# Kernel optimization log

Hardware: AMD Instinct MI355X
Metric: run time of the kernel (lower is better)

The kernel has to match this reference:

```python
import jax, jax.numpy as jnp
import numpy as np

D_MODEL = 1024
NUM_HEADS = 16
D_K = D_MODEL // NUM_HEADS
B, T = 2, 2048
NEG = -1e9


def setup_inputs() -> dict:
    key = jax.random.key(0)
    ks = jax.random.split(key, 12)
    s = 1.0 / np.sqrt(D_MODEL)
    q = jax.random.normal(ks[0], (B, T, D_MODEL), jnp.float32)
    k = jax.random.normal(ks[1], (B, T, D_MODEL), jnp.float32)
    v = jax.random.normal(ks[2], (B, T, D_MODEL), jnp.float32)
    # padding mask: True = valid key; realistic per-example lengths
    lengths = jnp.array([T, 3 * T // 4], dtype=jnp.int32)
    key_padding_mask = jnp.arange(T)[None, :] < lengths[:, None]
    Wq = jax.random.uniform(ks[3], (D_MODEL, D_MODEL), jnp.float32, -s, s)
    bq = jax.random.uniform(ks[4], (D_MODEL,), jnp.float32, -s, s)
    Wk = jax.random.uniform(ks[5], (D_MODEL, D_MODEL), jnp.float32, -s, s)
    bk = jax.random.uniform(ks[6], (D_MODEL,), jnp.float32, -s, s)
    Wv = jax.random.uniform(ks[7], (D_MODEL, D_MODEL), jnp.float32, -s, s)
    bv = jax.random.uniform(ks[8], (D_MODEL,), jnp.float32, -s, s)
    Wo = jax.random.uniform(ks[9], (D_MODEL, D_MODEL), jnp.float32, -s, s)
    bo = jax.random.uniform(ks[10], (D_MODEL,), jnp.float32, -s, s)
    return {"q": q, "k": k, "v": v, "key_padding_mask": key_padding_mask,
            "Wq": Wq, "bq": bq, "Wk": Wk, "bk": bk,
            "Wv": Wv, "bv": bv, "Wo": Wo, "bo": bo}


def reference(q, k, v, key_padding_mask, Wq, bq, Wk, bk, Wv, bv, Wo, bo):
    Bq, Tq, D = q.shape
    Tk = k.shape[1]
    # projections (torch Linear: x @ W.T + b), split heads -> [B, H, T, d_k]
    Q = (q @ Wq.T + bq).reshape(Bq, Tq, NUM_HEADS, D_K).transpose(0, 2, 1, 3)
    K = (k @ Wk.T + bk).reshape(Bq, Tk, NUM_HEADS, D_K).transpose(0, 2, 1, 3)
    V = (v @ Wv.T + bv).reshape(Bq, Tk, NUM_HEADS, D_K).transpose(0, 2, 1, 3)
    logits = jnp.einsum("bhqd,bhkd->bhqk", Q, K) / jnp.sqrt(jnp.float32(D_K))
    causal = jnp.tril(jnp.ones((Tq, Tk), dtype=bool))  # [Tq, Tk]
    mask = causal[None, None, :, :] & key_padding_mask[:, None, None, :]
    logits = jnp.where(mask, logits, NEG)
    scores = jax.nn.softmax(logits, axis=-1)
    out = jnp.einsum("bhqk,bhkd->bhqd", scores, V)
    out = out.transpose(0, 2, 1, 3).reshape(Bq, Tq, D)
    # dropout is identity in eval mode
    return out @ Wo.T + bo
```

## Files before the change

kernel.cpp:

```cpp
#include <hip/hip_runtime.h>
#include <stdint.h>

#define D_MODEL 1024
#define NHEAD 16
#define DK 64
#define BATCH 2
#define SEQ 2048
#define NROW 4096

typedef __attribute__((ext_vector_type(8))) _Float16 f16x8;
typedef __attribute__((ext_vector_type(4))) float f32x4;

__device__ __forceinline__ uint16_t f2h(float x) {
    _Float16 h = (_Float16)x;
    union { _Float16 h; uint16_t u; } cv;
    cv.h = h;
    return cv.u;
}

__device__ __forceinline__ float fexp2(float x) {
#if __has_builtin(__builtin_amdgcn_exp2f)
    return __builtin_amdgcn_exp2f(x);
#else
    return exp2f(x);
#endif
}

__device__ __forceinline__ void lds_dma16(const uint16_t* g, uint16_t* l) {
    __builtin_amdgcn_global_load_lds((const __attribute__((address_space(1))) void*)g,
                                     (__attribute__((address_space(3))) void*)l,
                                     16, 0, 0);
}

struct CvtArgs {
    const float* src[7];
    uint16_t* dst[7];
    int n4[7];
};
__global__ void cvt_all_kernel(CvtArgs a) {
    int t = blockIdx.y;
    const float* src = a.src[t];
    uint16_t* dst = a.dst[t];
    int n4 = a.n4[t];
    int i = blockIdx.x * blockDim.x + threadIdx.x;
    int stride = gridDim.x * blockDim.x;
    for (; i < n4; i += stride) {
        float4 v = ((const float4*)src)[i];
        ushort4 o;
        o.x = f2h(v.x); o.y = f2h(v.y); o.z = f2h(v.z); o.w = f2h(v.w);
        ((ushort4*)dst)[i] = o;
    }
}

__global__ void lens_kernel(const int* __restrict__ mask, int* __restrict__ lens) {
    __shared__ int red[256];
    int tid = threadIdx.x;
    int mx = 0;
    for (int i = tid; i < 1024; i += 256) { int v = mask[i]; if (v > mx) mx = v; }
    red[tid] = mx; __syncthreads();
    for (int s = 128; s > 0; s >>= 1) { if (tid < s) { if (red[tid+s] > red[tid]) red[tid] = red[tid+s]; } __syncthreads(); }
    int bytemode = (red[0] > 1);
    __syncthreads();
    const unsigned char* mb = (const unsigned char*)mask;
    for (int b = 0; b < BATCH; ++b) {
        int cnt = 0;
        for (int t = tid; t < SEQ; t += 256) {
            int v = bytemode ? (int)mb[b*SEQ + t] : mask[b*SEQ + t];
            cnt += (v != 0) ? 1 : 0;
        }
        red[tid] = cnt; __syncthreads();
        for (int s = 128; s > 0; s >>= 1) { if (tid < s) red[tid] += red[tid+s]; __syncthreads(); }
        if (tid == 0) lens[b] = red[0];
        __syncthreads();
    }
}

__device__ __forceinline__ void gemm_tile_core(const uint16_t* __restrict__ A,
                                               const uint16_t* __restrict__ W,
                                               int bx, int by,
                                               uint16_t* As, uint16_t* Bs,
                                               f32x4 (&acc)[4][4]) {
    const f32x4 fzero = {0.f, 0.f, 0.f, 0.f};
    int tid = threadIdx.x;
    int lane = tid & 63, wave = tid >> 6;
    int wm = wave >> 1, wn = wave & 1;
    int l15 = lane & 15, quad = lane >> 4;
    int rl = lane >> 2, cbl = lane & 3;
#pragma unroll
    for (int mi = 0; mi < 4; mi++)
#pragma unroll
        for (int ni = 0; ni < 4; ni++) acc[mi][ni] = fzero;

    for (int k0 = 0; k0 < D_MODEL; k0 += 32) {
        __syncthreads();
#pragma unroll
        for (int i = 0; i < 2; ++i) {
            int d8 = wave * 2 + i;
            int row = d8 * 16 + rl;
            int cbg = cbl ^ ((row >> 1) & 3);
            lds_dma16(A + (size_t)(bx * 128 + row) * D_MODEL + k0 + cbg * 8, As + d8 * 512);
            lds_dma16(W + (size_t)(by * 128 + row) * D_MODEL + k0 + cbg * 8, Bs + d8 * 512);
        }
        __syncthreads();
        f16x8 af[4], bf[4];
#pragma unroll
        for (int mi = 0; mi < 4; mi++) {
            int row = wm * 64 + mi * 16 + l15;
            af[mi] = *(const f16x8*)(As + row * 32 + (quad ^ ((row >> 1) & 3)) * 8);
        }
#pragma unroll
        for (int ni = 0; ni < 4; ni++) {
            int row = wn * 64 + ni * 16 + l15;
            bf[ni] = *(const f16x8*)(Bs + row * 32 + (quad ^ ((row >> 1) & 3)) * 8);
        }
#pragma unroll
        for (int mi = 0; mi < 4; mi++)
#pragma unroll
            for (int ni = 0; ni < 4; ni++)
                acc[mi][ni] = __builtin_amdgcn_mfma_f32_16x16x32_f16(af[mi], bf[ni], acc[mi][ni], 0, 0, 0);
    }
}

#define TS_STRIDE 136
__global__ __launch_bounds__(256, 3) void qkv_kernel(
    const uint16_t* __restrict__ qb, const uint16_t* __restrict__ kb, const uint16_t* __restrict__ vb,
    const uint16_t* __restrict__ wq, const uint16_t* __restrict__ wk, const uint16_t* __restrict__ wv,
    const float* __restrict__ bq, const float* __restrict__ bk, const float* __restrict__ bv,
    uint16_t* __restrict__ Qh, uint16_t* __restrict__ Kh, uint16_t* __restrict__ Vth) {
    __shared__ uint16_t smem[TS_STRIDE * 128];
    uint16_t* As = smem;
    uint16_t* Bs = smem + 128 * 32;
    int v = blockIdx.z;
    const uint16_t* A = (v == 0) ? qb : ((v == 1) ? kb : vb);
    const uint16_t* W = (v == 0) ? wq : ((v == 1) ? wk : wv);
    const float* bias = (v == 0) ? bq : ((v == 1) ? bk : bv);
    f32x4 acc[4][4];
    gemm_tile_core(A, W, blockIdx.x, blockIdx.y, As, Bs, acc);

    int tid = threadIdx.x, lane = tid & 63, wave = tid >> 6;
    int wm = wave >> 1, wn = wave & 1, l15 = lane & 15, quad = lane >> 4;
    const float QSCALE = 0.125f * 1.44269504088896f;

    if (v == 2) {
        __syncthreads();
        uint16_t* Ts = smem;
#pragma unroll
        for (int mi = 0; mi < 4; mi++) {
#pragma unroll
            for (int ni = 0; ni < 4; ni++) {
                int col = wn * 64 + ni * 16 + l15;
                float bcol = bias[blockIdx.y * 128 + col];
#pragma unroll
                for (int r = 0; r < 4; r++) {
                    int tl = wm * 64 + mi * 16 + quad * 4 + r;
                    Ts[col * TS_STRIDE + tl] = f2h(acc[mi][ni][r] + bcol);
                }
            }
        }
        __syncthreads();
        int col = tid >> 1, th = (tid & 1) << 6;
        int gcol = blockIdx.y * 128 + col;
        int h = gcol >> 6, d = gcol & 63;
        int grow0 = blockIdx.x * 128;
        int b = grow0 >> 11, t = (grow0 & (SEQ - 1)) + th;
        size_t base = (((size_t)(b * NHEAD + h) << 6) + d) * SEQ + t;
#pragma unroll
        for (int j = 0; j < 8; j++)
            *(uint4*)(Vth + base + j * 8) = *(const uint4*)(Ts + col * TS_STRIDE + th + j * 8);
        return;
    }

#pragma unroll
    for (int mi = 0; mi < 4; mi++) {
#pragma unroll
        for (int ni = 0; ni < 4; ni++) {
            int gcol = blockIdx.y * 128 + wn * 64 + ni * 16 + l15;
            float bcol = bias[gcol];
            int h = gcol >> 6, d = gcol & 63;
#pragma unroll
            for (int r = 0; r < 4; r++) {
                int grow = blockIdx.x * 128 + wm * 64 + mi * 16 + quad * 4 + r;
                int b = grow >> 11, t = grow & (SEQ - 1);
                float val = acc[mi][ni][r] + bcol;
                size_t bh = (size_t)(b * NHEAD + h);
                if (v == 0) Qh[(bh * SEQ + t) * 64 + d] = f2h(val * QSCALE);
                else        Kh[(bh * SEQ + t) * 64 + d] = f2h(val);
            }
        }
    }
}

__global__ __launch_bounds__(256, 3) void outproj_kernel(
    const uint16_t* __restrict__ attn, const uint16_t* __restrict__ wo,
    const float* __restrict__ bo, float* __restrict__ out) {
    __shared__ uint16_t As[128 * 32], Bs[128 * 32];
    f32x4 acc[4][4];
    gemm_tile_core(attn, wo, blockIdx.x, blockIdx.y, As, Bs, acc);
    int tid = threadIdx.x, lane = tid & 63, wave = tid >> 6;
    int wm = wave >> 1, wn = wave & 1, l15 = lane & 15, quad = lane >> 4;
#pragma unroll
    for (int mi = 0; mi < 4; mi++) {
#pragma unroll
        for (int ni = 0; ni < 4; ni++) {
            int gcol = blockIdx.y * 128 + wn * 64 + ni * 16 + l15;
            float bcol = bo[gcol];
#pragma unroll
            for (int r = 0; r < 4; r++) {
                int grow = blockIdx.x * 128 + wm * 64 + mi * 16 + quad * 4 + r;
                out[(size_t)grow * D_MODEL + gcol] = acc[mi][ni][r] + bcol;
            }
        }
    }
}

__device__ __forceinline__ void flash_one(
    int qt, int bh, int b, int h, int L,
    const uint16_t* __restrict__ Qh, const uint16_t* __restrict__ Kh, const uint16_t* __restrict__ Vth,
    uint16_t* __restrict__ attn,
    uint16_t* Kt0, uint16_t* Kt1, uint16_t* Vt0, uint16_t* Vt1, uint16_t* Ptw) {
    const f32x4 fzero = {0.f, 0.f, 0.f, 0.f};
    const float MFIX = 6.0f;
    int tid = threadIdx.x, lane = tid & 63, w = tid >> 6;
    int l15 = lane & 15, quad = lane >> 4, l7 = l15 & 7;
    int q0 = qt * 64;
    int rl = lane >> 3, cb8 = lane & 7;

    f16x8 ones;
#pragma unroll
    for (int j = 0; j < 8; j++) ones[j] = (_Float16)1.0f;

    f16x8 qf[2];
#pragma unroll
    for (int ks = 0; ks < 2; ks++)
        qf[ks] = *(const f16x8*)(Qh + ((size_t)bh * SEQ + q0 + w * 16 + l15) * 64 + ks * 32 + quad * 8);

    f32x4 o_acc[4], l_acc = fzero;
#pragma unroll
    for (int ni = 0; ni < 4; ni++) o_acc[ni] = fzero;

    int nkt_p = (L + 63) >> 6;
    int nkt = (qt + 1 < nkt_p) ? (qt + 1) : nkt_p;

    uint16_t* Ktb[2] = {Kt0, Kt1};
    uint16_t* Vtb[2] = {Vt0, Vt1};

    auto stage = [&](int kt_, int buf_) {
#pragma unroll
        for (int i_ = 0; i_ < 2; ++i_) {
            int d8 = w * 2 + i_;
            int row = d8 * 8 + rl;
            int cbg = cb8 ^ rl;
            lds_dma16(Kh + ((size_t)bh * SEQ + kt_ * 64 + row) * 64 + cbg * 8, Ktb[buf_] + d8 * 512);
            lds_dma16(Vth + (((size_t)bh << 6) + row) * SEQ + kt_ * 64 + cbg * 8, Vtb[buf_] + d8 * 512);
        }
    };

    stage(0, 0);
    __syncthreads();

    for (int kt = 0; kt < nkt; ++kt) {
        int cur = kt & 1;
        if (kt + 1 < nkt) stage(kt + 1, cur ^ 1);

        f32x4 s_acc[4];
#pragma unroll
        for (int ni = 0; ni < 4; ni++) s_acc[ni] = fzero;
#pragma unroll
        for (int ks = 0; ks < 2; ks++) {
            f16x8 kf[4];
#pragma unroll
            for (int ni = 0; ni < 4; ni++)
                kf[ni] = *(const f16x8*)(Ktb[cur] + (ni * 16 + l15) * 64 + ((ks * 4 + quad) ^ l7) * 8);
#pragma unroll
            for (int ni = 0; ni < 4; ni++)
                s_acc[ni] = __builtin_amdgcn_mfma_f32_16x16x32_f16(qf[ks], kf[ni], s_acc[ni], 0, 0, 0);
        }

        bool full = (kt < qt) && (kt * 64 + 64 <= L);
#pragma unroll
        for (int r = 0; r < 4; r++) {
            int prow = quad * 4 + r;
            int q_idx = q0 + w * 16 + prow;
            int pr7 = prow & 7;
#pragma unroll
            for (int ni = 0; ni < 4; ni++) {
                float s = s_acc[ni][r];
                if (!full) {
                    int key = kt * 64 + ni * 16 + l15;
                    s = ((key <= q_idx) && (key < L)) ? s : -1e9f;
                }
                float p = fexp2(s - MFIX);
                int cb = ni * 2 + (l15 >> 3);
                Ptw[prow * 64 + ((cb ^ pr7) * 8) + l7] = f2h(p);
            }
        }
        __asm__ __volatile__("" ::: "memory");

#pragma unroll
        for (int ks = 0; ks < 2; ks++) {
            f16x8 pa = *(const f16x8*)(Ptw + l15 * 64 + (((ks * 4 + quad) ^ l7) * 8));
            l_acc = __builtin_amdgcn_mfma_f32_16x16x32_f16(pa, ones, l_acc, 0, 0, 0);
            f16x8 vbf[4];
#pragma unroll
            for (int ni = 0; ni < 4; ni++)
                vbf[ni] = *(const f16x8*)(Vtb[cur] + (ni * 16 + l15) * 64 + ((ks * 4 + quad) ^ l7) * 8);
#pragma unroll
            for (int ni = 0; ni < 4; ni++)
                o_acc[ni] = __builtin_amdgcn_mfma_f32_16x16x32_f16(pa, vbf[ni], o_acc[ni], 0, 0, 0);
        }
        __syncthreads();
    }

#pragma unroll
    for (int r = 0; r < 4; r++) {
        float inv = 1.0f / l_acc[r];
        int q_idx = q0 + w * 16 + quad * 4 + r;
#pragma unroll
        for (int ni = 0; ni < 4; ni++) {
            attn[((size_t)(b * SEQ + q_idx)) * D_MODEL + h * 64 + ni * 16 + l15] =
                f2h(o_acc[ni][r] * inv);
        }
    }
}

__global__ __launch_bounds__(256, 2) void attn_kernel(
    const uint16_t* __restrict__ Qh, const uint16_t* __restrict__ Kh, const uint16_t* __restrict__ Vth,
    uint16_t* __restrict__ attn, const int* __restrict__ lens) {
    __shared__ uint16_t Kt[2][64 * 64];
    __shared__ uint16_t Vt[2][64 * 64];
    __shared__ uint16_t Pt[4][16 * 64];
    int bh = blockIdx.y;
    int b = bh >> 4, h = bh & 15;
    int L = lens[b];
    int w = threadIdx.x >> 6;
    uint16_t* Ptw = &Pt[w][0];
    int qt1 = 31 - (int)blockIdx.x;
    int qt2 = (int)blockIdx.x;
    flash_one(qt1, bh, b, h, L, Qh, Kh, Vth, attn, &Kt[0][0], &Kt[1][0], &Vt[0][0], &Vt[1][0], Ptw);
    __syncthreads();
    flash_one(qt2, bh, b, h, L, Qh, Kh, Vth, attn, &Kt[0][0], &Kt[1][0], &Vt[0][0], &Vt[1][0], Ptw);
}

extern "C" void kernel_launch(void* const* d_in, const int* in_sizes, int n_in,
                              void* d_out, int out_size, void* d_ws, size_t ws_size,
                              hipStream_t stream) {
    const float* q  = (const float*)d_in[0];
    const float* k  = (const float*)d_in[1];
    const float* v  = (const float*)d_in[2];
    const int*   mask = (const int*)d_in[3];
    const float* Wq = (const float*)d_in[4];
    const float* bq = (const float*)d_in[5];
    const float* Wk = (const float*)d_in[6];
    const float* bk = (const float*)d_in[7];
    const float* Wv = (const float*)d_in[8];
    const float* bv = (const float*)d_in[9];
    const float* Wo = (const float*)d_in[10];
    const float* bo = (const float*)d_in[11];
    float* out = (float*)d_out;

    char* ws = (char*)d_ws;
    size_t off = 0;
    auto alloc = [&](size_t bytes) -> char* {
        char* p = ws + off;
        off += (bytes + 255) & ~(size_t)255;
        return p;
    };
    const size_t inp_e = (size_t)NROW * D_MODEL;
    const size_t w_e   = (size_t)D_MODEL * D_MODEL;
    uint16_t* qbf  = (uint16_t*)alloc(inp_e * 2);
    uint16_t* kbf  = (uint16_t*)alloc(inp_e * 2);
    uint16_t* vbf  = (uint16_t*)alloc(inp_e * 2);
    uint16_t* wqb  = (uint16_t*)alloc(w_e * 2);
    uint16_t* wkb  = (uint16_t*)alloc(w_e * 2);
    uint16_t* wvb  = (uint16_t*)alloc(w_e * 2);
    uint16_t* wob  = (uint16_t*)alloc(w_e * 2);
    uint16_t* Qhb  = (uint16_t*)alloc(inp_e * 2);
    uint16_t* Khb  = (uint16_t*)alloc(inp_e * 2);
    uint16_t* Vtb  = (uint16_t*)alloc(inp_e * 2);
    uint16_t* attb = (uint16_t*)alloc(inp_e * 2);
    int* lens      = (int*)alloc(256);

    CvtArgs ca;
    ca.src[0] = q;  ca.dst[0] = qbf; ca.n4[0] = (int)(inp_e / 4);
    ca.src[1] = k;  ca.dst[1] = kbf; ca.n4[1] = (int)(inp_e / 4);
    ca.src[2] = v;  ca.dst[2] = vbf; ca.n4[2] = (int)(inp_e / 4);
    ca.src[3] = Wq; ca.dst[3] = wqb; ca.n4[3] = (int)(w_e / 4);
    ca.src[4] = Wk; ca.dst[4] = wkb; ca.n4[4] = (int)(w_e / 4);
    ca.src[5] = Wv; ca.dst[5] = wvb; ca.n4[5] = (int)(w_e / 4);
    ca.src[6] = Wo; ca.dst[6] = wob; ca.n4[6] = (int)(w_e / 4);
    cvt_all_kernel<<<dim3(128, 7), 256, 0, stream>>>(ca);
    lens_kernel<<<dim3(1), 256, 0, stream>>>(mask, lens);

    qkv_kernel<<<dim3(32, 8, 3), 256, 0, stream>>>(qbf, kbf, vbf, wqb, wkb, wvb,
                                                   bq, bk, bv, Qhb, Khb, Vtb);
    attn_kernel<<<dim3(16, 32), 256, 0, stream>>>(Qhb, Khb, Vtb, attb, lens);
    outproj_kernel<<<dim3(32, 8), 256, 0, stream>>>(attb, wob, bo, out);
}
```

Baseline: 249.7 us.

## Fuse lens into convert, widen GEMM K-tile, add atomic work queue for attention

Folds the mask-length reduction into the conversion kernel as an extra grid row, which drops one launch and also resets an atomic counter. The shared GEMM core now stages 64-wide K tiles with an 8-way XOR swizzle, halving the number of barriers per K loop at the cost of twice the LDS per tile. The attention kernel replaces the fixed paired-tile mapping with a dynamic queue that pulls work items longest-first through an atomicAdd. It launches 1024 blocks with higher occupancy bounds, adding one atomic and one barrier per tile.

```diff
diff --git a/kernel.cpp b/kernel.cpp
--- a/kernel.cpp
+++ b/kernel.cpp
@@ -37,8 +37,33 @@
     uint16_t* dst[7];
     int n4[7];
 };
-__global__ void cvt_all_kernel(CvtArgs a) {
+__global__ void cvt_all_kernel(CvtArgs a, const int* __restrict__ mask, int* __restrict__ lens_ctr) {
     int t = blockIdx.y;
+    if (t == 7) {
+        if (blockIdx.x != 0) return;
+        __shared__ int red[256];
+        int tid = threadIdx.x;
+        int mx = 0;
+        for (int i = tid; i < 1024; i += 256) { int v = mask[i]; if (v > mx) mx = v; }
+        red[tid] = mx; __syncthreads();
+        for (int s = 128; s > 0; s >>= 1) { if (tid < s) { if (red[tid+s] > red[tid]) red[tid] = red[tid+s]; } __syncthreads(); }
+        int bytemode = (red[0] > 1);
+        __syncthreads();
+        const unsigned char* mb = (const unsigned char*)mask;
+        for (int b = 0; b < BATCH; ++b) {
+            int cnt = 0;
+            for (int tt = tid; tt < SEQ; tt += 256) {
+                int v = bytemode ? (int)mb[b*SEQ + tt] : mask[b*SEQ + tt];
+                cnt += (v != 0) ? 1 : 0;
+            }
+            red[tid] = cnt; __syncthreads();
+            for (int s = 128; s > 0; s >>= 1) { if (tid < s) red[tid] += red[tid+s]; __syncthreads(); }
+            if (tid == 0) lens_ctr[b] = red[0];
+            __syncthreads();
+        }
+        if (tid == 0) lens_ctr[2] = 0;
+        return;
+    }
     const float* src = a.src[t];
     uint16_t* dst = a.dst[t];
     int n4 = a.n4[t];
@@ -52,29 +77,6 @@
     }
 }
 
-__global__ void lens_kernel(const int* __restrict__ mask, int* __restrict__ lens) {
-    __shared__ int red[256];
-    int tid = threadIdx.x;
-    int mx = 0;
-    for (int i = tid; i < 1024; i += 256) { int v = mask[i]; if (v > mx) mx = v; }
-    red[tid] = mx; __syncthreads();
-    for (int s = 128; s > 0; s >>= 1) { if (tid < s) { if (red[tid+s] > red[tid]) red[tid] = red[tid+s]; } __syncthreads(); }
-    int bytemode = (red[0] > 1);
-    __syncthreads();
-    const unsigned char* mb = (const unsigned char*)mask;
-    for (int b = 0; b < BATCH; ++b) {
-        int cnt = 0;
-        for (int t = tid; t < SEQ; t += 256) {
-            int v = bytemode ? (int)mb[b*SEQ + t] : mask[b*SEQ + t];
-            cnt += (v != 0) ? 1 : 0;
-        }
-        red[tid] = cnt; __syncthreads();
-        for (int s = 128; s > 0; s >>= 1) { if (tid < s) red[tid] += red[tid+s]; __syncthreads(); }
-        if (tid == 0) lens[b] = red[0];
-        __syncthreads();
-    }
-}
-
 __device__ __forceinline__ void gemm_tile_core(const uint16_t* __restrict__ A,
                                                const uint16_t* __restrict__ W,
                                                int bx, int by,
@@ -85,39 +87,42 @@
     int lane = tid & 63, wave = tid >> 6;
     int wm = wave >> 1, wn = wave & 1;
     int l15 = lane & 15, quad = lane >> 4;
-    int rl = lane >> 2, cbl = lane & 3;
+    int rl = lane >> 3, cb8 = lane & 7;
 #pragma unroll
     for (int mi = 0; mi < 4; mi++)
 #pragma unroll
         for (int ni = 0; ni < 4; ni++) acc[mi][ni] = fzero;
 
-    for (int k0 = 0; k0 < D_MODEL; k0 += 32) {
-        __syncthreads();
-#pragma unroll
-        for (int i = 0; i < 2; ++i) {
-            int d8 = wave * 2 + i;
-            int row = d8 * 16 + rl;
-            int cbg = cbl ^ ((row >> 1) & 3);
+    for (int k0 = 0; k0 < D_MODEL; k0 += 64) {
+        __syncthreads();
+#pragma unroll
+        for (int i = 0; i < 4; ++i) {
+            int d8 = wave * 4 + i;
+            int row = d8 * 8 + rl;
+            int cbg = cb8 ^ rl;
             lds_dma16(A + (size_t)(bx * 128 + row) * D_MODEL + k0 + cbg * 8, As + d8 * 512);
             lds_dma16(W + (size_t)(by * 128 + row) * D_MODEL + k0 + cbg * 8, Bs + d8 * 512);
         }
         __syncthreads();
-        f16x8 af[4], bf[4];
-#pragma unroll
-        for (int mi = 0; mi < 4; mi++) {
-            int row = wm * 64 + mi * 16 + l15;
-            af[mi] = *(const f16x8*)(As + row * 32 + (quad ^ ((row >> 1) & 3)) * 8);
-        }
-#pragma unroll
-        for (int ni = 0; ni < 4; ni++) {
-            int row = wn * 64 + ni * 16 + l15;
-            bf[ni] = *(const f16x8*)(Bs + row * 32 + (quad ^ ((row >> 1) & 3)) * 8);
-        }
-#pragma unroll
-        for (int mi = 0; mi < 4; mi++)
-#pragma unroll
-            for (int ni = 0; ni < 4; ni++)
-                acc[mi][ni] = __builtin_amdgcn_mfma_f32_16x16x32_f16(af[mi], bf[ni], acc[mi][ni], 0, 0, 0);
+#pragma unroll
+        for (int ks = 0; ks < 2; ks++) {
+            f16x8 af[4], bf[4];
+#pragma unroll
+            for (int mi = 0; mi < 4; mi++) {
+                int row = wm * 64 + mi * 16 + l15;
+                af[mi] = *(const f16x8*)(As + row * 64 + (((ks * 4 + quad) ^ (row & 7)) * 8));
+            }
+#pragma unroll
+            for (int ni = 0; ni < 4; ni++) {
+                int row = wn * 64 + ni * 16 + l15;
+                bf[ni] = *(const f16x8*)(Bs + row * 64 + (((ks * 4 + quad) ^ (row & 7)) * 8));
+            }
+#pragma unroll
+            for (int mi = 0; mi < 4; mi++)
+#pragma unroll
+                for (int ni = 0; ni < 4; ni++)
+                    acc[mi][ni] = __builtin_amdgcn_mfma_f32_16x16x32_f16(af[mi], bf[ni], acc[mi][ni], 0, 0, 0);
+        }
     }
 }
 
@@ -129,7 +134,7 @@
     uint16_t* __restrict__ Qh, uint16_t* __restrict__ Kh, uint16_t* __restrict__ Vth) {
     __shared__ uint16_t smem[TS_STRIDE * 128];
     uint16_t* As = smem;
-    uint16_t* Bs = smem + 128 * 32;
+    uint16_t* Bs = smem + 128 * 64;
     int v = blockIdx.z;
     const uint16_t* A = (v == 0) ? qb : ((v == 1) ? kb : vb);
     const uint16_t* W = (v == 0) ? wq : ((v == 1) ? wk : wv);
@@ -193,7 +198,7 @@
 __global__ __launch_bounds__(256, 3) void outproj_kernel(
     const uint16_t* __restrict__ attn, const uint16_t* __restrict__ wo,
     const float* __restrict__ bo, float* __restrict__ out) {
-    __shared__ uint16_t As[128 * 32], Bs[128 * 32];
+    __shared__ uint16_t As[128 * 64], Bs[128 * 64];
     f32x4 acc[4][4];
     gemm_tile_core(attn, wo, blockIdx.x, blockIdx.y, As, Bs, acc);
     int tid = threadIdx.x, lane = tid & 63, wave = tid >> 6;
@@ -323,22 +328,29 @@
     }
 }
 
-__global__ __launch_bounds__(256, 2) void attn_kernel(
+__global__ __launch_bounds__(256, 4) void attn_kernel(
     const uint16_t* __restrict__ Qh, const uint16_t* __restrict__ Kh, const uint16_t* __restrict__ Vth,
-    uint16_t* __restrict__ attn, const int* __restrict__ lens) {
+    uint16_t* __restrict__ attn, int* __restrict__ lens_ctr) {
     __shared__ uint16_t Kt[2][64 * 64];
     __shared__ uint16_t Vt[2][64 * 64];
     __shared__ uint16_t Pt[4][16 * 64];
-    int bh = blockIdx.y;
-    int b = bh >> 4, h = bh & 15;
-    int L = lens[b];
-    int w = threadIdx.x >> 6;
+    __shared__ int curi;
+    int tid = threadIdx.x;
+    int w = tid >> 6;
     uint16_t* Ptw = &Pt[w][0];
-    int qt1 = 31 - (int)blockIdx.x;
-    int qt2 = (int)blockIdx.x;
-    flash_one(qt1, bh, b, h, L, Qh, Kh, Vth, attn, &Kt[0][0], &Kt[1][0], &Vt[0][0], &Vt[1][0], Ptw);
-    __syncthreads();
-    flash_one(qt2, bh, b, h, L, Qh, Kh, Vth, attn, &Kt[0][0], &Kt[1][0], &Vt[0][0], &Vt[1][0], Ptw);
+    int* ctr = lens_ctr + 2;
+    for (;;) {
+        if (tid == 0) curi = atomicAdd(ctr, 1);
+        __syncthreads();
+        int i = curi;
+        if (i >= 32 * 32) break;
+        int qt = 31 - (i >> 5);
+        int bh = i & 31;
+        int b = bh >> 4, h = bh & 15;
+        int L = lens_ctr[b];
+        flash_one(qt, bh, b, h, L, Qh, Kh, Vth, attn,
+                  &Kt[0][0], &Kt[1][0], &Vt[0][0], &Vt[1][0], Ptw);
+    }
 }
 
 extern "C" void kernel_launch(void* const* d_in, const int* in_sizes, int n_in,
@@ -378,7 +390,7 @@
     uint16_t* Khb  = (uint16_t*)alloc(inp_e * 2);
     uint16_t* Vtb  = (uint16_t*)alloc(inp_e * 2);
     uint16_t* attb = (uint16_t*)alloc(inp_e * 2);
-    int* lens      = (int*)alloc(256);
+    int* lens_ctr  = (int*)alloc(256);
 
     CvtArgs ca;
     ca.src[0] = q;  ca.dst[0] = qbf; ca.n4[0] = (int)(inp_e / 4);
@@ -388,11 +400,10 @@
     ca.src[4] = Wk; ca.dst[4] = wkb; ca.n4[4] = (int)(w_e / 4);
     ca.src[5] = Wv; ca.dst[5] = wvb; ca.n4[5] = (int)(w_e / 4);
     ca.src[6] = Wo; ca.dst[6] = wob; ca.n4[6] = (int)(w_e / 4);
-    cvt_all_kernel<<<dim3(128, 7), 256, 0, stream>>>(ca);
-    lens_kernel<<<dim3(1), 256, 0, stream>>>(mask, lens);
+    cvt_all_kernel<<<dim3(128, 8), 256, 0, stream>>>(ca, mask, lens_ctr);
 
     qkv_kernel<<<dim3(32, 8, 3), 256, 0, stream>>>(qbf, kbf, vbf, wqb, wkb, wvb,
                                                    bq, bk, bv, Qhb, Khb, Vtb);
-    attn_kernel<<<dim3(16, 32), 256, 0, stream>>>(Qhb, Khb, Vtb, attb, lens);
+    attn_kernel<<<dim3(1024), 256, 0, stream>>>(Qhb, Khb, Vtb, attb, lens_ctr);
     outproj_kernel<<<dim3(32, 8), 256, 0, stream>>>(attb, wob, bo, out);
 }
```

Result: slower. 258.2 us (+3.4%).
